# Performance work log

Hardware: AMD Instinct MI355X
Metric: run time of the kernel (lower is better)

The kernel has to match this reference:

```python
import jax, jax.numpy as jnp
import numpy as np

B, S, IN, D, H, L, M = 8, 1024, 256, 512, 8, 2, 64
DK = D // H
FF = 4 * D
EPS = 1e-5


def setup_inputs() -> dict:
    key = jax.random.key(0)
    ks = jax.random.split(key, 16)
    w = lambda k, shape: jax.random.normal(k, shape, jnp.float32) * 0.02
    return {
        "inputs": jax.random.normal(ks[0], (B, S, IN), jnp.float32),
        "lengths": jax.random.randint(ks[1], (B,), S // 2, S + 1),
        "W_in": w(ks[2], (IN, D)), "b_in": jnp.zeros((D,), jnp.float32),
        # per-layer stacked params (leading axis L) for lax.scan
        "Wq": w(ks[3], (L, D, D)), "bq": jnp.zeros((L, D), jnp.float32),
        "Wk": w(ks[4], (L, D, D)), "bk": jnp.zeros((L, D), jnp.float32),
        "Wv": w(ks[5], (L, D, D)), "bv": jnp.zeros((L, D), jnp.float32),
        "Wo": w(ks[6], (L, D, D)), "bo": jnp.zeros((L, D), jnp.float32),
        "rel_bias": w(ks[7], (L, H, 2 * M - 1)),
        "W1": w(ks[8], (L, D, FF)), "b1": jnp.zeros((L, FF), jnp.float32),
        "W2": w(ks[9], (L, FF, D)), "b2": jnp.zeros((L, D), jnp.float32),
        "g1": jnp.ones((L, D), jnp.float32), "be1": jnp.zeros((L, D), jnp.float32),
        "g2": jnp.ones((L, D), jnp.float32), "be2": jnp.zeros((L, D), jnp.float32),
        "gf": jnp.ones((D,), jnp.float32), "bef": jnp.zeros((D,), jnp.float32),
    }


def _ln(x, g, b):
    m = jnp.mean(x, axis=-1, keepdims=True)
    v = jnp.mean(jnp.square(x - m), axis=-1, keepdims=True)
    return (x - m) * jax.lax.rsqrt(v + EPS) * g + b


def _sinusoid_pe(seq_len, d_model):
    pos = jnp.arange(seq_len, dtype=jnp.float32)[:, None]
    div = jnp.exp(jnp.arange(0, d_model, 2, dtype=jnp.float32) * (-np.log(10000.0) / d_model))
    pe = jnp.zeros((seq_len, d_model), jnp.float32)
    pe = pe.at[:, 0::2].set(jnp.sin(pos * div))
    pe = pe.at[:, 1::2].set(jnp.cos(pos * div))
    return pe


def _encoder(inputs, lengths, W_in, b_in, Wq, bq, Wk, bk, Wv, bv, Wo, bo,
             rel_bias, W1, b1, W2, b2, g1, be1, g2, be2, gf, bef):
    x = inputs @ W_in + b_in                      # (B,S,D)
    x = x + _sinusoid_pe(S, D)[None]
    pad = jnp.arange(S)[None, :] >= lengths[:, None]   # (B,S) True = padded key

    r = jnp.arange(S)
    rel_idx = jnp.clip(r[:, None] - r[None, :], -(M - 1), M - 1) + (M - 1)  # (S,S)
    scale = 1.0 / np.sqrt(DK)

    def layer(x, p):
        (wq, bq_, wk, bk_, wv, bv_, wo, bo_, rb, w1, b1_, w2, b2_, g1_, be1_, g2_, be2_) = p
        # --- self-attention sublayer (pre-norm) ---
        h = _ln(x, g1_, be1_)
        q = (h @ wq + bq_).reshape(B, S, H, DK).transpose(0, 2, 1, 3)  # (B,H,S,DK)
        k = (h @ wk + bk_).reshape(B, S, H, DK).transpose(0, 2, 1, 3)
        v = (h @ wv + bv_).reshape(B, S, H, DK).transpose(0, 2, 1, 3)
        scores = jnp.einsum('bhqd,bhkd->bhqk', q, k) * scale
        scores = scores + rb[:, rel_idx][None]            # (H,S,S) relative bias
        scores = jnp.where(pad[:, None, None, :], -jnp.inf, scores)
        attn = jax.nn.softmax(scores, axis=-1)
        o = jnp.einsum('bhqk,bhkd->bhqd', attn, v)
        o = o.transpose(0, 2, 1, 3).reshape(B, S, D) @ wo + bo_
        x = x + o
        # --- FFN sublayer (pre-norm) ---
        h = _ln(x, g2_, be2_)
        x = x + (jax.nn.relu(h @ w1 + b1_) @ w2 + b2_)
        return x, None

    stacked = (Wq, bq, Wk, bk, Wv, bv, Wo, bo, rel_bias, W1, b1, W2, b2, g1, be1, g2, be2)
    x, _ = jax.lax.scan(layer, x, stacked)
    return _ln(x, gf, bef)


def reference(inputs, lengths, W_in, b_in, Wq, bq, Wk, bk, Wv, bv, Wo, bo,
              rel_bias, W1, b1, W2, b2, g1, be1, g2, be2, gf, bef):
    return _encoder(inputs, lengths, W_in, b_in, Wq, bq, Wk, bk, Wv, bv, Wo, bo,
                    rel_bias, W1, b1, W2, b2, g1, be1, g2, be2, gf, bef)
```

## Files before the change

### kernel.cpp

```cpp
#include <hip/hip_runtime.h>
#include <hip/hip_bf16.h>

typedef unsigned short u16;
typedef unsigned int u32;
typedef __bf16 v8bf __attribute__((ext_vector_type(8)));
typedef float v4f __attribute__((ext_vector_type(4)));

#define B_SZ 8
#define S_LEN 1024
#define IN_DIM 256
#define DMODEL 512
#define NHEAD 8
#define DK 64
#define FF_DIM 2048
#define MROWS (B_SZ * S_LEN)
#define QSCALE 0.1803368801111204f

__device__ __forceinline__ u16 f2bf(float f) {
    unsigned int x = __float_as_uint(f);
    unsigned int r = (x + 0x7fffu + ((x >> 16) & 1u)) >> 16;
    return (u16)r;
}

__device__ __forceinline__ void gl16(const u16* g, u16* l) {
    __builtin_amdgcn_global_load_lds((const __attribute__((address_space(1))) unsigned int*)g,
                                     (__attribute__((address_space(3))) unsigned int*)l, 16, 0, 0);
}

__global__ __launch_bounds__(256) void conv_bf16_kernel(const float* __restrict__ in,
                                                        u16* __restrict__ out, int n4) {
    int i = blockIdx.x * 256 + threadIdx.x;
    if (i < n4) {
        float4 v = ((const float4*)in)[i];
        ushort4 o;
        o.x = f2bf(v.x); o.y = f2bf(v.y); o.z = f2bf(v.z); o.w = f2bf(v.w);
        ((ushort4*)out)[i] = o;
    }
}

struct TDesc { const float* src; u16* dst; int K; int N; };
struct TArgs { TDesc d[13]; };

__global__ void transpose_conv_kernel(TArgs args) {
    TDesc t = args.d[blockIdx.z];
    int k0 = blockIdx.x * 32, n0 = blockIdx.y * 32;
    if (k0 >= t.K || n0 >= t.N) return;
    __shared__ float tile[32][33];
    int tx = threadIdx.x, ty = threadIdx.y;
#pragma unroll
    for (int j = 0; j < 4; j++) {
        int k = k0 + ty + j * 8;
        tile[ty + j * 8][tx] = t.src[(size_t)k * t.N + n0 + tx];
    }
    __syncthreads();
#pragma unroll
    for (int j = 0; j < 4; j++) {
        int n = n0 + ty + j * 8;
        t.dst[(size_t)n * t.K + k0 + tx] = f2bf(tile[tx][ty + j * 8]);
    }
}

template <bool OUT_BF16>
__global__ __launch_bounds__(256) void ln_kernel(const float* __restrict__ x,
                                                 const float* __restrict__ g,
                                                 const float* __restrict__ b,
                                                 void* __restrict__ out) {
    int row = blockIdx.x * 4 + (threadIdx.x >> 6);
    int lane = threadIdx.x & 63;
    const float4* xr = (const float4*)(x + (size_t)row * DMODEL);
    float4 v0 = xr[lane], v1 = xr[lane + 64];
    float s = v0.x + v0.y + v0.z + v0.w + v1.x + v1.y + v1.z + v1.w;
    float sq = v0.x * v0.x + v0.y * v0.y + v0.z * v0.z + v0.w * v0.w +
               v1.x * v1.x + v1.y * v1.y + v1.z * v1.z + v1.w * v1.w;
#pragma unroll
    for (int m = 1; m < 64; m <<= 1) {
        s += __shfl_xor(s, m);
        sq += __shfl_xor(sq, m);
    }
    float mean = s * (1.0f / DMODEL);
    float var = sq * (1.0f / DMODEL) - mean * mean;
    float rstd = rsqrtf(var + 1e-5f);
    const float4* g4 = (const float4*)g;
    const float4* b4 = (const float4*)b;
    float4 ga = g4[lane], gb = g4[lane + 64], ba = b4[lane], bb = b4[lane + 64];
    float4 r0, r1;
    r0.x = (v0.x - mean) * rstd * ga.x + ba.x;
    r0.y = (v0.y - mean) * rstd * ga.y + ba.y;
    r0.z = (v0.z - mean) * rstd * ga.z + ba.z;
    r0.w = (v0.w - mean) * rstd * ga.w + ba.w;
    r1.x = (v1.x - mean) * rstd * gb.x + bb.x;
    r1.y = (v1.y - mean) * rstd * gb.y + bb.y;
    r1.z = (v1.z - mean) * rstd * gb.z + bb.z;
    r1.w = (v1.w - mean) * rstd * gb.w + bb.w;
    if (OUT_BF16) {
        ushort4 o0, o1;
        o0.x = f2bf(r0.x); o0.y = f2bf(r0.y); o0.z = f2bf(r0.z); o0.w = f2bf(r0.w);
        o1.x = f2bf(r1.x); o1.y = f2bf(r1.y); o1.z = f2bf(r1.z); o1.w = f2bf(r1.w);
        ((ushort4*)out)[(size_t)row * 128 + lane] = o0;
        ((ushort4*)out)[(size_t)row * 128 + 64 + lane] = o1;
    } else {
        ((float4*)out)[(size_t)row * 128 + lane] = r0;
        ((float4*)out)[(size_t)row * 128 + 64 + lane] = r1;
    }
}

template <int MT, int NT>
__device__ __forceinline__ void gemm_core(const u16* __restrict__ A, const u16* __restrict__ Bt,
                                          int K, v4f (&acc)[MT][NT]) {
    constexpr int BM = MT * 32;
    constexpr int BN = NT * 32;
    __shared__ u16 As[BM * 64];
    __shared__ u16 Bs[BN * 64];
    int tid = threadIdx.x;
    int n0 = blockIdx.x * BN, m0 = blockIdx.y * BM;
    int w = tid >> 6, lane = tid & 63;
    int wr = (w >> 1) * (BM / 2), wc = (w & 1) * (BN / 2);
    int lr = lane & 15, lq = lane >> 4;
    int r8 = lane >> 3, cb = lane & 7;
    int scol = (cb ^ r8) * 8;

    v4f zero = {0.f, 0.f, 0.f, 0.f};
#pragma unroll
    for (int i = 0; i < MT; i++)
#pragma unroll
        for (int j = 0; j < NT; j++) acc[i][j] = zero;

    const u16* gA[MT]; u16* lA[MT];
#pragma unroll
    for (int j = 0; j < MT; j++) {
        int row0 = (MT * 8) * w + j * 8;
        gA[j] = A + (size_t)(m0 + row0 + r8) * K + scol;
        lA[j] = As + row0 * 64;
    }
    const u16* gB[NT]; u16* lB[NT];
#pragma unroll
    for (int j = 0; j < NT; j++) {
        int row0 = (NT * 8) * w + j * 8;
        gB[j] = Bt + (size_t)(n0 + row0 + r8) * K + scol;
        lB[j] = Bs + row0 * 64;
    }

    for (int k0 = 0; k0 < K; k0 += 64) {
#pragma unroll
        for (int j = 0; j < MT; j++) gl16(gA[j], lA[j]);
#pragma unroll
        for (int j = 0; j < NT; j++) gl16(gB[j], lB[j]);
        __syncthreads();
#pragma unroll
        for (int kk = 0; kk < 2; kk++) {
            int xb = ((kk * 4 + lq) ^ (lr & 7)) * 8;
            v8bf af[MT], bfr[NT];
#pragma unroll
            for (int i = 0; i < MT; i++)
                af[i] = *(const v8bf*)&As[(wr + i * 16 + lr) * 64 + xb];
#pragma unroll
            for (int j = 0; j < NT; j++)
                bfr[j] = *(const v8bf*)&Bs[(wc + j * 16 + lr) * 64 + xb];
#pragma unroll
            for (int mt = 0; mt < MT; mt++)
#pragma unroll
                for (int nt = 0; nt < NT; nt++)
                    acc[mt][nt] = __builtin_amdgcn_mfma_f32_16x16x32_bf16(af[mt], bfr[nt], acc[mt][nt], 0, 0, 0);
        }
        __syncthreads();
#pragma unroll
        for (int j = 0; j < MT; j++) gA[j] += 64;
#pragma unroll
        for (int j = 0; j < NT; j++) gB[j] += 64;
    }
}

__global__ __launch_bounds__(256) void gemm_in_kernel(const u16* __restrict__ A,
                                                      const u16* __restrict__ Bt,
                                                      const float* __restrict__ bias,
                                                      float* __restrict__ Out, int K) {
    v4f acc[4][2];
    gemm_core<4, 2>(A, Bt, K, acc);
    int tid = threadIdx.x, w = tid >> 6, lane = tid & 63;
    int lr = lane & 15, lq = lane >> 4;
    int wr = (w >> 1) * 64, wc = (w & 1) * 32;
    int n0 = blockIdx.x * 64, m0 = blockIdx.y * 128;
#pragma unroll
    for (int mt = 0; mt < 4; mt++) {
#pragma unroll
        for (int nt = 0; nt < 2; nt++) {
            int col = n0 + wc + nt * 16 + lr;
            float bcol = bias[col];
            float freq = __builtin_amdgcn_exp2f((float)(col & ~1) * (-0.025953277f));
#pragma unroll
            for (int reg = 0; reg < 4; reg++) {
                int row = m0 + wr + mt * 16 + lq * 4 + reg;
                float rev = (float)(row & (S_LEN - 1)) * freq * 0.15915494309189535f;
                float fr = __builtin_amdgcn_fractf(rev);
                float pe = (col & 1) ? __builtin_amdgcn_cosf(fr) : __builtin_amdgcn_sinf(fr);
                Out[(size_t)row * DMODEL + col] = acc[mt][nt][reg] + bcol + pe;
            }
        }
    }
}

__global__ __launch_bounds__(256) void gemm_qkv_kernel(const u16* __restrict__ A,
                                                       const u16* __restrict__ Bt,
                                                       const float* __restrict__ bq,
                                                       const float* __restrict__ bk,
                                                       const float* __restrict__ bv,
                                                       u16* __restrict__ Qo,
                                                       u16* __restrict__ Ko,
                                                       u16* __restrict__ Vto, int K) {
    v4f acc[4][4];
    gemm_core<4, 4>(A, Bt, K, acc);
    int tid = threadIdx.x, w = tid >> 6, lane = tid & 63;
    int lr = lane & 15, lq = lane >> 4;
    int wr = (w >> 1) * 64, wc = (w & 1) * 64;
    int n0 = blockIdx.x * 128, m0 = blockIdx.y * 128;
    int seg = n0 >> 9;
#pragma unroll
    for (int mt = 0; mt < 4; mt++) {
#pragma unroll
        for (int nt = 0; nt < 4; nt++) {
            int col = (n0 + wc + nt * 16 + lr) & (DMODEL - 1);
            if (seg == 0) {
                float bcol = bq[col];
#pragma unroll
                for (int reg = 0; reg < 4; reg++) {
                    int row = m0 + wr + mt * 16 + lq * 4 + reg;
                    Qo[(size_t)row * DMODEL + col] = f2bf((acc[mt][nt][reg] + bcol) * QSCALE);
                }
            } else if (seg == 1) {
                float bcol = bk[col];
#pragma unroll
                for (int reg = 0; reg < 4; reg++) {
                    int row = m0 + wr + mt * 16 + lq * 4 + reg;
                    Ko[(size_t)row * DMODEL + col] = f2bf(acc[mt][nt][reg] + bcol);
                }
            } else {
                float bcol = bv[col];
                int row0 = m0 + wr + mt * 16 + lq * 4;
                int bb = row0 >> 10, s0 = row0 & (S_LEN - 1);
                ushort4 o;
                o.x = f2bf(acc[mt][nt][0] + bcol);
                o.y = f2bf(acc[mt][nt][1] + bcol);
                o.z = f2bf(acc[mt][nt][2] + bcol);
                o.w = f2bf(acc[mt][nt][3] + bcol);
                *(ushort4*)(Vto + ((size_t)(bb * DMODEL + col)) * S_LEN + s0) = o;
            }
        }
    }
}

__global__ __launch_bounds__(256) void gemm_relu_kernel(const u16* __restrict__ A,
                                                        const u16* __restrict__ Bt,
                                                        const float* __restrict__ bias,
                                                        u16* __restrict__ Out, int N, int K) {
    v4f acc[4][4];
    gemm_core<4, 4>(A, Bt, K, acc);
    int tid = threadIdx.x, w = tid >> 6, lane = tid & 63;
    int lr = lane & 15, lq = lane >> 4;
    int wr = (w >> 1) * 64, wc = (w & 1) * 64;
    int n0 = blockIdx.x * 128, m0 = blockIdx.y * 128;
#pragma unroll
    for (int mt = 0; mt < 4; mt++) {
#pragma unroll
        for (int nt = 0; nt < 4; nt++) {
            int col = n0 + wc + nt * 16 + lr;
            float bcol = bias[col];
#pragma unroll
            for (int reg = 0; reg < 4; reg++) {
                int row = m0 + wr + mt * 16 + lq * 4 + reg;
                Out[(size_t)row * N + col] = f2bf(fmaxf(acc[mt][nt][reg] + bcol, 0.0f));
            }
        }
    }
}

__global__ __launch_bounds__(256) void gemm_res_kernel(const u16* __restrict__ A,
                                                       const u16* __restrict__ Bt,
                                                       const float* __restrict__ bias,
                                                       float* __restrict__ Out, int K) {
    v4f acc[4][2];
    gemm_core<4, 2>(A, Bt, K, acc);
    int tid = threadIdx.x, w = tid >> 6, lane = tid & 63;
    int lr = lane & 15, lq = lane >> 4;
    int wr = (w >> 1) * 64, wc = (w & 1) * 32;
    int n0 = blockIdx.x * 64, m0 = blockIdx.y * 128;
#pragma unroll
    for (int mt = 0; mt < 4; mt++) {
#pragma unroll
        for (int nt = 0; nt < 2; nt++) {
            int col = n0 + wc + nt * 16 + lr;
            float bcol = bias[col];
#pragma unroll
            for (int reg = 0; reg < 4; reg++) {
                int row = m0 + wr + mt * 16 + lq * 4 + reg;
                size_t idx = (size_t)row * DMODEL + col;
                Out[idx] = Out[idx] + acc[mt][nt][reg] + bcol;
            }
        }
    }
}

__global__ __launch_bounds__(256, 4) void fattn_kernel(const u16* __restrict__ Qg,
                                                       const u16* __restrict__ Kg,
                                                       const u16* __restrict__ Vtg,
                                                       const float* __restrict__ rb,
                                                       const int* __restrict__ lengths,
                                                       u16* __restrict__ Op,
                                                       float* __restrict__ lsums) {
    int bid = blockIdx.x;
    int wg = (bid & 7) * 128 + (bid >> 3);
    int i = wg & 127;
    int h = wg >> 7;
    int b = i & 7;
    int qt = (i >> 3) & 7;
    int kvh = (i >> 6) & 1;
    int tid = threadIdx.x, w = tid >> 6, lane = tid & 63;
    int lr = lane & 15, lq = lane >> 4;
    __shared__ u16 Ks[3][64 * 64];
    __shared__ u16 Vs[3][64 * 64];
    __shared__ float rbs[128];
    int len = lengths[b];
    if (tid < 127) rbs[tid] = rb[h * 127 + tid] * 1.4426950408889634f;

    int l2 = ((len + 127) >> 7) << 6;
    int kstart = kvh ? l2 : 0;
    int kend = kvh ? len : l2;
    int nchunks = (kend - kstart + 63) >> 6;

    int qw = qt * 128 + w * 32;
    v8bf qa[2][2];
#pragma unroll
    for (int ntq = 0; ntq < 2; ntq++) {
        size_t qrow = ((size_t)(b * S_LEN + qw + ntq * 16 + lr)) * DMODEL + h * DK;
        qa[ntq][0] = *(const v8bf*)(Qg + qrow + lq * 8);
        qa[ntq][1] = *(const v8bf*)(Qg + qrow + 32 + lq * 8);
    }

    v4f zero = {0.f, 0.f, 0.f, 0.f};
    v4f Oacc[4][2];
#pragma unroll
    for (int dt = 0; dt < 4; dt++)
#pragma unroll
        for (int nt = 0; nt < 2; nt++) Oacc[dt][nt] = zero;
    float lsum[2] = {0.f, 0.f};

    const u16* Kbase = Kg + ((size_t)b * S_LEN) * DMODEL + h * DK;
    const u16* Vbase = Vtg + ((size_t)(b * DMODEL + h * DK)) * S_LEN;
    int r8 = lane >> 3, cb = lane & 7;
    int swz = (cb ^ r8) * 8;

#pragma unroll
    for (int j = 0; j < 2; j++) {
        int row0 = w * 16 + j * 8;
        gl16(Kbase + (size_t)(kstart + row0 + r8) * DMODEL + swz, Ks[0] + row0 * 64);
        gl16(Vbase + (size_t)(row0 + r8) * S_LEN + kstart + swz, Vs[0] + row0 * 64);
    }
#pragma unroll
    for (int j = 0; j < 2; j++) {
        int row0 = w * 16 + j * 8;
        gl16(Kbase + (size_t)(kstart + 64 + row0 + r8) * DMODEL + swz, Ks[1] + row0 * 64);
        gl16(Vbase + (size_t)(row0 + r8) * S_LEN + kstart + 64 + swz, Vs[1] + row0 * 64);
    }
    __syncthreads();

    u16 *KsA = Ks[0], *VsA = Vs[0];
    u16 *KsB = Ks[1], *VsB = Vs[1];
    u16 *KsC = Ks[2], *VsC = Vs[2];

    for (int ci = 0; ci < nchunks; ci++) {
        int kb0 = kstart + ci * 64;
        if (ci > 0) {
            if (ci + 1 < nchunks) asm volatile("s_waitcnt vmcnt(4)" ::: "memory");
            else                  asm volatile("s_waitcnt vmcnt(0)" ::: "memory");
            __builtin_amdgcn_s_barrier();
            __builtin_amdgcn_sched_barrier(0);
        }
        if (ci + 2 < nchunks) {
            int nk = kb0 + 128;
#pragma unroll
            for (int j = 0; j < 2; j++) {
                int row0 = w * 16 + j * 8;
                gl16(Kbase + (size_t)(nk + row0 + r8) * DMODEL + swz, KsC + row0 * 64);
                gl16(Vbase + (size_t)(row0 + r8) * S_LEN + nk + swz, VsC + row0 * 64);
            }
        }
        const u16* Ksc = KsA;
        const u16* Vsc = VsA;

        v4f S[4][2];
        __builtin_amdgcn_s_setprio(1);
#pragma unroll
        for (int mtk = 0; mtk < 4; mtk++) {
            int xb0 = (lq ^ (lr & 7)) * 8;
            int xb1 = ((4 + lq) ^ (lr & 7)) * 8;
            v8bf kf0 = *(const v8bf*)&Ksc[(mtk * 16 + lr) * 64 + xb0];
            v8bf kf1 = *(const v8bf*)&Ksc[(mtk * 16 + lr) * 64 + xb1];
#pragma unroll
            for (int ntq = 0; ntq < 2; ntq++) {
                v4f s = __builtin_amdgcn_mfma_f32_16x16x32_bf16(kf0, qa[ntq][0], zero, 0, 0, 0);
                S[mtk][ntq] = __builtin_amdgcn_mfma_f32_16x16x32_bf16(kf1, qa[ntq][1], s, 0, 0, 0);
            }
        }
        __builtin_amdgcn_s_setprio(0);

        bool edge = (kb0 + 64 > len);
        int dmin = qw - (kb0 + 63), dmax = qw + 31 - kb0;
        bool perel = !(dmax <= -63 || dmin >= 63);
        float bconst = (dmax <= -63) ? rbs[0] : rbs[126];
        uint2 pks[4][2];
#pragma unroll
        for (int mtk = 0; mtk < 4; mtk++) {
#pragma unroll
            for (int ntq = 0; ntq < 2; ntq++) {
                int q = qw + ntq * 16 + lr;
                float p[4];
#pragma unroll
                for (int r = 0; r < 4; r++) {
                    int key = kb0 + mtk * 16 + lq * 4 + r;
                    float s = S[mtk][ntq][r];
                    if (perel) {
                        int d = q - key;
                        d = d < -63 ? -63 : (d > 63 ? 63 : d);
                        s += rbs[d + 63];
                    } else {
                        s += bconst;
                    }
                    float pv = __builtin_amdgcn_exp2f(s);
                    if (edge && key >= len) pv = 0.f;
                    lsum[ntq] += pv;
                    p[r] = pv;
                }
                pks[mtk][ntq].x = (__float_as_uint(p[1]) & 0xffff0000u) | (__float_as_uint(p[0]) >> 16);
                pks[mtk][ntq].y = (__float_as_uint(p[3]) & 0xffff0000u) | (__float_as_uint(p[2]) >> 16);
            }
        }

        __builtin_amdgcn_s_setprio(1);
#pragma unroll
        for (int kh = 0; kh < 2; kh++) {
            uint4 tp0 = {pks[kh * 2][0].x, pks[kh * 2][0].y, pks[kh * 2 + 1][0].x, pks[kh * 2 + 1][0].y};
            uint4 tp1 = {pks[kh * 2][1].x, pks[kh * 2][1].y, pks[kh * 2 + 1][1].x, pks[kh * 2 + 1][1].y};
            v8bf pb0 = *(v8bf*)&tp0;
            v8bf pb1 = *(v8bf*)&tp1;
            int gl = kh * 4 + (lq >> 1);
            int sub = (lq & 1) * 4;
#pragma unroll
            for (int dt = 0; dt < 4; dt++) {
                int drow = (dt * 16 + lr) * 64;
                uint2 lo = *(const uint2*)&Vsc[drow + ((gl ^ (lr & 7)) * 8 + sub)];
                uint2 hi = *(const uint2*)&Vsc[drow + (((gl + 2) ^ (lr & 7)) * 8 + sub)];
                uint4 tv = {lo.x, lo.y, hi.x, hi.y};
                v8bf va = *(v8bf*)&tv;
                Oacc[dt][0] = __builtin_amdgcn_mfma_f32_16x16x32_bf16(va, pb0, Oacc[dt][0], 0, 0, 0);
                Oacc[dt][1] = __builtin_amdgcn_mfma_f32_16x16x32_bf16(va, pb1, Oacc[dt][1], 0, 0, 0);
            }
        }
        __builtin_amdgcn_s_setprio(0);

        u16* t;
        t = KsA; KsA = KsB; KsB = KsC; KsC = t;
        t = VsA; VsA = VsB; VsB = VsC; VsC = t;
    }

    float lsumR[2];
#pragma unroll
    for (int ntq = 0; ntq < 2; ntq++) {
        float s = lsum[ntq];
        s += __shfl_xor(s, 16);
        s += __shfl_xor(s, 32);
        lsumR[ntq] = s;
    }
    if (lq == 0) {
#pragma unroll
        for (int ntq = 0; ntq < 2; ntq++) {
            int q = qw + ntq * 16 + lr;
            lsums[((size_t)kvh * MROWS + b * S_LEN + q) * NHEAD + h] = lsumR[ntq];
        }
    }
    u16* Oh = Op + (size_t)kvh * MROWS * DMODEL;
#pragma unroll
    for (int dt = 0; dt < 4; dt++) {
#pragma unroll
        for (int ntq = 0; ntq < 2; ntq++) {
            size_t off = (size_t)(b * S_LEN + qw + ntq * 16 + lr) * DMODEL + h * DK + dt * 16 + lq * 4;
            ushort4 o;
            o.x = f2bf(Oacc[dt][ntq][0]);
            o.y = f2bf(Oacc[dt][ntq][1]);
            o.z = f2bf(Oacc[dt][ntq][2]);
            o.w = f2bf(Oacc[dt][ntq][3]);
            *(ushort4*)(Oh + off) = o;
        }
    }
}

__device__ __forceinline__ u32 comb2(u32 a, u32 b, float inv) {
    float r0 = (__uint_as_float(a << 16) + __uint_as_float(b << 16)) * inv;
    float r1 = (__uint_as_float(a & 0xffff0000u) + __uint_as_float(b & 0xffff0000u)) * inv;
    return (u32)f2bf(r0) | ((u32)f2bf(r1) << 16);
}

__global__ __launch_bounds__(256) void attn_combine_kernel(const u16* __restrict__ Op,
                                                           const float* __restrict__ lsums,
                                                           u16* __restrict__ out) {
    int row = blockIdx.x * 4 + (threadIdx.x >> 6);
    int lane = threadIdx.x & 63;
    int h = lane >> 3;
    float l0 = lsums[(size_t)row * NHEAD + h];
    float l1 = lsums[((size_t)MROWS + row) * NHEAD + h];
    float inv = 1.0f / (l0 + l1);
    size_t base = (size_t)row * DMODEL + lane * 8;
    uint4 a = *(const uint4*)(Op + base);
    uint4 c = *(const uint4*)(Op + (size_t)MROWS * DMODEL + base);
    uint4 o;
    o.x = comb2(a.x, c.x, inv);
    o.y = comb2(a.y, c.y, inv);
    o.z = comb2(a.z, c.z, inv);
    o.w = comb2(a.w, c.w, inv);
    *(uint4*)(out + base) = o;
}

extern "C" void kernel_launch(void* const* d_in, const int* in_sizes, int n_in,
                              void* d_out, int out_size, void* d_ws, size_t ws_size,
                              hipStream_t stream) {
    const float* inputs   = (const float*)d_in[0];
    const int*   lengths  = (const int*)d_in[1];
    const float* W_in     = (const float*)d_in[2];
    const float* b_in     = (const float*)d_in[3];
    const float* Wq       = (const float*)d_in[4];
    const float* bq       = (const float*)d_in[5];
    const float* Wk       = (const float*)d_in[6];
    const float* bk       = (const float*)d_in[7];
    const float* Wv       = (const float*)d_in[8];
    const float* bv       = (const float*)d_in[9];
    const float* Wo       = (const float*)d_in[10];
    const float* bo       = (const float*)d_in[11];
    const float* rel_bias = (const float*)d_in[12];
    const float* W1       = (const float*)d_in[13];
    const float* b1       = (const float*)d_in[14];
    const float* W2       = (const float*)d_in[15];
    const float* b2       = (const float*)d_in[16];
    const float* g1       = (const float*)d_in[17];
    const float* be1      = (const float*)d_in[18];
    const float* g2       = (const float*)d_in[19];
    const float* be2      = (const float*)d_in[20];
    const float* gf       = (const float*)d_in[21];
    const float* bef      = (const float*)d_in[22];

    char* ws = (char*)d_ws;
    float* xbuf = (float*)ws;          ws += (size_t)MROWS * DMODEL * 4;
    u16* hbuf   = (u16*)ws;            ws += (size_t)MROWS * DMODEL * 2;
    u16* aobuf  = hbuf;
    u16* qbf    = (u16*)ws;            ws += (size_t)MROWS * FF_DIM * 2;
    u16* kbf    = qbf + (size_t)MROWS * DMODEL;
    u16* vtbf   = kbf + (size_t)MROWS * DMODEL;
    float* lsums = (float*)(vtbf + (size_t)MROWS * DMODEL);
    u16* tbuf   = qbf;
    u16* inbf   = qbf;
    u16* opart  = (u16*)d_out;
    u16* wt_in  = (u16*)ws;            ws += (size_t)DMODEL * IN_DIM * 2;
    u16 *qkvw[2], *wto[2], *wt1[2], *wt2[2];
    for (int l = 0; l < 2; l++) { qkvw[l] = (u16*)ws; ws += (size_t)3 * DMODEL * DMODEL * 2; }
    for (int l = 0; l < 2; l++) { wto[l] = (u16*)ws; ws += (size_t)DMODEL * DMODEL * 2; }
    for (int l = 0; l < 2; l++) { wt1[l] = (u16*)ws; ws += (size_t)FF_DIM * DMODEL * 2; }
    for (int l = 0; l < 2; l++) { wt2[l] = (u16*)ws; ws += (size_t)DMODEL * FF_DIM * 2; }

    TArgs ta;
    int ti = 0;
    ta.d[ti++] = {W_in, wt_in, IN_DIM, DMODEL};
    for (int l = 0; l < 2; l++) {
        ta.d[ti++] = {Wq + (size_t)l * DMODEL * DMODEL, qkvw[l], DMODEL, DMODEL};
        ta.d[ti++] = {Wk + (size_t)l * DMODEL * DMODEL, qkvw[l] + (size_t)DMODEL * DMODEL, DMODEL, DMODEL};
        ta.d[ti++] = {Wv + (size_t)l * DMODEL * DMODEL, qkvw[l] + (size_t)2 * DMODEL * DMODEL, DMODEL, DMODEL};
        ta.d[ti++] = {Wo + (size_t)l * DMODEL * DMODEL, wto[l], DMODEL, DMODEL};
        ta.d[ti++] = {W1 + (size_t)l * DMODEL * FF_DIM, wt1[l], DMODEL, FF_DIM};
        ta.d[ti++] = {W2 + (size_t)l * FF_DIM * DMODEL, wt2[l], FF_DIM, DMODEL};
    }

    conv_bf16_kernel<<<dim3((MROWS * IN_DIM / 4 + 255) / 256), 256, 0, stream>>>(
        inputs, inbf, MROWS * IN_DIM / 4);
    transpose_conv_kernel<<<dim3(64, 64, 13), dim3(32, 8), 0, stream>>>(ta);

    gemm_in_kernel<<<dim3(DMODEL / 64, MROWS / 128), 256, 0, stream>>>(
        inbf, wt_in, b_in, xbuf, IN_DIM);

    for (int l = 0; l < 2; l++) {
        ln_kernel<true><<<MROWS / 4, 256, 0, stream>>>(xbuf, g1 + l * DMODEL, be1 + l * DMODEL, hbuf);
        gemm_qkv_kernel<<<dim3(3 * DMODEL / 128, MROWS / 128), 256, 0, stream>>>(
            hbuf, qkvw[l], bq + l * DMODEL, bk + l * DMODEL, bv + l * DMODEL,
            qbf, kbf, vtbf, DMODEL);
        fattn_kernel<<<dim3(1024), 256, 0, stream>>>(
            qbf, kbf, vtbf, rel_bias + (size_t)l * NHEAD * 127, lengths, opart, lsums);
        attn_combine_kernel<<<MROWS / 4, 256, 0, stream>>>(opart, lsums, aobuf);
        gemm_res_kernel<<<dim3(DMODEL / 64, MROWS / 128), 256, 0, stream>>>(
            aobuf, wto[l], bo + l * DMODEL, xbuf, DMODEL);
        ln_kernel<true><<<MROWS / 4, 256, 0, stream>>>(xbuf, g2 + l * DMODEL, be2 + l * DMODEL, hbuf);
        gemm_relu_kernel<<<dim3(FF_DIM / 128, MROWS / 128), 256, 0, stream>>>(
            hbuf, wt1[l], b1 + l * FF_DIM, tbuf, FF_DIM, DMODEL);
        gemm_res_kernel<<<dim3(DMODEL / 64, MROWS / 128), 256, 0, stream>>>(
            tbuf, wt2[l], b2 + l * DMODEL, xbuf, FF_DIM);
    }
    ln_kernel<false><<<MROWS / 4, 256, 0, stream>>>(xbuf, gf, bef, d_out);
}
```

Baseline: 468.3 us.

## Drop split-KV attention and combine kernel; compact transpose grid

The attention kernel no longer splits the key range into two halves with a separate combine pass. Each workgroup now covers all keys and normalizes its output directly, which removes the combine kernel launch and the partial-output and lsum traffic. The cost is half as many workgroups (512) with longer, unevenly sized loops, so load balance and occupancy may suffer. The weight transpose launch also changes from a mostly idle 3D grid to a flat grid of only the valid tiles, found by a per-block search over start offsets.

```diff
diff --git a/kernel.cpp b/kernel.cpp
--- a/kernel.cpp
+++ b/kernel.cpp
@@ -39,12 +39,17 @@
 }
 
 struct TDesc { const float* src; u16* dst; int K; int N; };
-struct TArgs { TDesc d[13]; };
+struct TArgs { TDesc d[13]; int start[14]; int l2tn[13]; };
 
 __global__ void transpose_conv_kernel(TArgs args) {
-    TDesc t = args.d[blockIdx.z];
-    int k0 = blockIdx.x * 32, n0 = blockIdx.y * 32;
-    if (k0 >= t.K || n0 >= t.N) return;
+    int bid = blockIdx.x;
+    int z = 0;
+    while (z < 12 && bid >= args.start[z + 1]) z++;
+    TDesc t = args.d[z];
+    int local = bid - args.start[z];
+    int l2 = args.l2tn[z];
+    int k0 = (local >> l2) << 5;
+    int n0 = (local & ((1 << l2) - 1)) << 5;
     __shared__ float tile[32][33];
     int tx = threadIdx.x, ty = threadIdx.y;
 #pragma unroll
@@ -304,15 +309,13 @@
                                                        const u16* __restrict__ Vtg,
                                                        const float* __restrict__ rb,
                                                        const int* __restrict__ lengths,
-                                                       u16* __restrict__ Op,
-                                                       float* __restrict__ lsums) {
+                                                       u16* __restrict__ O) {
     int bid = blockIdx.x;
-    int wg = (bid & 7) * 128 + (bid >> 3);
-    int i = wg & 127;
-    int h = wg >> 7;
+    int wg = (bid & 7) * 64 + (bid >> 3);
+    int i = wg & 63;
+    int h = wg >> 6;
     int b = i & 7;
     int qt = (i >> 3) & 7;
-    int kvh = (i >> 6) & 1;
     int tid = threadIdx.x, w = tid >> 6, lane = tid & 63;
     int lr = lane & 15, lq = lane >> 4;
     __shared__ u16 Ks[3][64 * 64];
@@ -321,10 +324,7 @@
     int len = lengths[b];
     if (tid < 127) rbs[tid] = rb[h * 127 + tid] * 1.4426950408889634f;
 
-    int l2 = ((len + 127) >> 7) << 6;
-    int kstart = kvh ? l2 : 0;
-    int kend = kvh ? len : l2;
-    int nchunks = (kend - kstart + 63) >> 6;
+    int nchunks = (len + 63) >> 6;
 
     int qw = qt * 128 + w * 32;
     v8bf qa[2][2];
@@ -351,14 +351,14 @@
 #pragma unroll
     for (int j = 0; j < 2; j++) {
         int row0 = w * 16 + j * 8;
-        gl16(Kbase + (size_t)(kstart + row0 + r8) * DMODEL + swz, Ks[0] + row0 * 64);
-        gl16(Vbase + (size_t)(row0 + r8) * S_LEN + kstart + swz, Vs[0] + row0 * 64);
+        gl16(Kbase + (size_t)(row0 + r8) * DMODEL + swz, Ks[0] + row0 * 64);
+        gl16(Vbase + (size_t)(row0 + r8) * S_LEN + swz, Vs[0] + row0 * 64);
     }
 #pragma unroll
     for (int j = 0; j < 2; j++) {
         int row0 = w * 16 + j * 8;
-        gl16(Kbase + (size_t)(kstart + 64 + row0 + r8) * DMODEL + swz, Ks[1] + row0 * 64);
-        gl16(Vbase + (size_t)(row0 + r8) * S_LEN + kstart + 64 + swz, Vs[1] + row0 * 64);
+        gl16(Kbase + (size_t)(64 + row0 + r8) * DMODEL + swz, Ks[1] + row0 * 64);
+        gl16(Vbase + (size_t)(row0 + r8) * S_LEN + 64 + swz, Vs[1] + row0 * 64);
     }
     __syncthreads();
 
@@ -367,7 +367,7 @@
     u16 *KsC = Ks[2], *VsC = Vs[2];
 
     for (int ci = 0; ci < nchunks; ci++) {
-        int kb0 = kstart + ci * 64;
+        int kb0 = ci * 64;
         if (ci > 0) {
             if (ci + 1 < nchunks) asm volatile("s_waitcnt vmcnt(4)" ::: "memory");
             else                  asm volatile("s_waitcnt vmcnt(0)" ::: "memory");
@@ -461,61 +461,27 @@
         t = VsA; VsA = VsB; VsB = VsC; VsC = t;
     }
 
-    float lsumR[2];
+    float inv[2];
 #pragma unroll
     for (int ntq = 0; ntq < 2; ntq++) {
         float s = lsum[ntq];
         s += __shfl_xor(s, 16);
         s += __shfl_xor(s, 32);
-        lsumR[ntq] = s;
-    }
-    if (lq == 0) {
-#pragma unroll
-        for (int ntq = 0; ntq < 2; ntq++) {
-            int q = qw + ntq * 16 + lr;
-            lsums[((size_t)kvh * MROWS + b * S_LEN + q) * NHEAD + h] = lsumR[ntq];
-        }
-    }
-    u16* Oh = Op + (size_t)kvh * MROWS * DMODEL;
+        inv[ntq] = 1.0f / s;
+    }
 #pragma unroll
     for (int dt = 0; dt < 4; dt++) {
 #pragma unroll
         for (int ntq = 0; ntq < 2; ntq++) {
             size_t off = (size_t)(b * S_LEN + qw + ntq * 16 + lr) * DMODEL + h * DK + dt * 16 + lq * 4;
             ushort4 o;
-            o.x = f2bf(Oacc[dt][ntq][0]);
-            o.y = f2bf(Oacc[dt][ntq][1]);
-            o.z = f2bf(Oacc[dt][ntq][2]);
-            o.w = f2bf(Oacc[dt][ntq][3]);
-            *(ushort4*)(Oh + off) = o;
-        }
-    }
-}
-
-__device__ __forceinline__ u32 comb2(u32 a, u32 b, float inv) {
-    float r0 = (__uint_as_float(a << 16) + __uint_as_float(b << 16)) * inv;
-    float r1 = (__uint_as_float(a & 0xffff0000u) + __uint_as_float(b & 0xffff0000u)) * inv;
-    return (u32)f2bf(r0) | ((u32)f2bf(r1) << 16);
-}
-
-__global__ __launch_bounds__(256) void attn_combine_kernel(const u16* __restrict__ Op,
-                                                           const float* __restrict__ lsums,
-                                                           u16* __restrict__ out) {
-    int row = blockIdx.x * 4 + (threadIdx.x >> 6);
-    int lane = threadIdx.x & 63;
-    int h = lane >> 3;
-    float l0 = lsums[(size_t)row * NHEAD + h];
-    float l1 = lsums[((size_t)MROWS + row) * NHEAD + h];
-    float inv = 1.0f / (l0 + l1);
-    size_t base = (size_t)row * DMODEL + lane * 8;
-    uint4 a = *(const uint4*)(Op + base);
-    uint4 c = *(const uint4*)(Op + (size_t)MROWS * DMODEL + base);
-    uint4 o;
-    o.x = comb2(a.x, c.x, inv);
-    o.y = comb2(a.y, c.y, inv);
-    o.z = comb2(a.z, c.z, inv);
-    o.w = comb2(a.w, c.w, inv);
-    *(uint4*)(out + base) = o;
+            o.x = f2bf(Oacc[dt][ntq][0] * inv[ntq]);
+            o.y = f2bf(Oacc[dt][ntq][1] * inv[ntq]);
+            o.z = f2bf(Oacc[dt][ntq][2] * inv[ntq]);
+            o.w = f2bf(Oacc[dt][ntq][3] * inv[ntq]);
+            *(ushort4*)(O + off) = o;
+        }
+    }
 }
 
 extern "C" void kernel_launch(void* const* d_in, const int* in_sizes, int n_in,
@@ -552,10 +518,8 @@
     u16* qbf    = (u16*)ws;            ws += (size_t)MROWS * FF_DIM * 2;
     u16* kbf    = qbf + (size_t)MROWS * DMODEL;
     u16* vtbf   = kbf + (size_t)MROWS * DMODEL;
-    float* lsums = (float*)(vtbf + (size_t)MROWS * DMODEL);
     u16* tbuf   = qbf;
     u16* inbf   = qbf;
-    u16* opart  = (u16*)d_out;
     u16* wt_in  = (u16*)ws;            ws += (size_t)DMODEL * IN_DIM * 2;
     u16 *qkvw[2], *wto[2], *wt1[2], *wt2[2];
     for (int l = 0; l < 2; l++) { qkvw[l] = (u16*)ws; ws += (size_t)3 * DMODEL * DMODEL * 2; }
@@ -564,20 +528,30 @@
     for (int l = 0; l < 2; l++) { wt2[l] = (u16*)ws; ws += (size_t)DMODEL * FF_DIM * 2; }
 
     TArgs ta;
-    int ti = 0;
-    ta.d[ti++] = {W_in, wt_in, IN_DIM, DMODEL};
+    int ti = 0, acct = 0;
+    auto add = [&](const float* s, u16* d, int K, int N) {
+        ta.d[ti] = {s, d, K, N};
+        ta.start[ti] = acct;
+        int tn = N / 32;
+        int l2 = 31 - __builtin_clz((unsigned)tn);
+        ta.l2tn[ti] = l2;
+        acct += (K / 32) * tn;
+        ti++;
+    };
+    add(W_in, wt_in, IN_DIM, DMODEL);
     for (int l = 0; l < 2; l++) {
-        ta.d[ti++] = {Wq + (size_t)l * DMODEL * DMODEL, qkvw[l], DMODEL, DMODEL};
-        ta.d[ti++] = {Wk + (size_t)l * DMODEL * DMODEL, qkvw[l] + (size_t)DMODEL * DMODEL, DMODEL, DMODEL};
-        ta.d[ti++] = {Wv + (size_t)l * DMODEL * DMODEL, qkvw[l] + (size_t)2 * DMODEL * DMODEL, DMODEL, DMODEL};
-        ta.d[ti++] = {Wo + (size_t)l * DMODEL * DMODEL, wto[l], DMODEL, DMODEL};
-        ta.d[ti++] = {W1 + (size_t)l * DMODEL * FF_DIM, wt1[l], DMODEL, FF_DIM};
-        ta.d[ti++] = {W2 + (size_t)l * FF_DIM * DMODEL, wt2[l], FF_DIM, DMODEL};
-    }
+        add(Wq + (size_t)l * DMODEL * DMODEL, qkvw[l], DMODEL, DMODEL);
+        add(Wk + (size_t)l * DMODEL * DMODEL, qkvw[l] + (size_t)DMODEL * DMODEL, DMODEL, DMODEL);
+        add(Wv + (size_t)l * DMODEL * DMODEL, qkvw[l] + (size_t)2 * DMODEL * DMODEL, DMODEL, DMODEL);
+        add(Wo + (size_t)l * DMODEL * DMODEL, wto[l], DMODEL, DMODEL);
+        add(W1 + (size_t)l * DMODEL * FF_DIM, wt1[l], DMODEL, FF_DIM);
+        add(W2 + (size_t)l * FF_DIM * DMODEL, wt2[l], FF_DIM, DMODEL);
+    }
+    ta.start[13] = acct;
 
     conv_bf16_kernel<<<dim3((MROWS * IN_DIM / 4 + 255) / 256), 256, 0, stream>>>(
         inputs, inbf, MROWS * IN_DIM / 4);
-    transpose_conv_kernel<<<dim3(64, 64, 13), dim3(32, 8), 0, stream>>>(ta);
+    transpose_conv_kernel<<<dim3(acct), dim3(32, 8), 0, stream>>>(ta);
 
     gemm_in_kernel<<<dim3(DMODEL / 64, MROWS / 128), 256, 0, stream>>>(
         inbf, wt_in, b_in, xbuf, IN_DIM);
@@ -587,9 +561,8 @@
         gemm_qkv_kernel<<<dim3(3 * DMODEL / 128, MROWS / 128), 256, 0, stream>>>(
             hbuf, qkvw[l], bq + l * DMODEL, bk + l * DMODEL, bv + l * DMODEL,
             qbf, kbf, vtbf, DMODEL);
-        fattn_kernel<<<dim3(1024), 256, 0, stream>>>(
-            qbf, kbf, vtbf, rel_bias + (size_t)l * NHEAD * 127, lengths, opart, lsums);
-        attn_combine_kernel<<<MROWS / 4, 256, 0, stream>>>(opart, lsums, aobuf);
+        fattn_kernel<<<dim3(512), 256, 0, stream>>>(
+            qbf, kbf, vtbf, rel_bias + (size_t)l * NHEAD * 127, lengths, aobuf);
         gemm_res_kernel<<<dim3(DMODEL / 64, MROWS / 128), 256, 0, stream>>>(
             aobuf, wto[l], bo + l * DMODEL, xbuf, DMODEL);
         ln_kernel<true><<<MROWS / 4, 256, 0, stream>>>(xbuf, g2 + l * DMODEL, be2 + l * DMODEL, hbuf);
```

New measurement: 444.8 us. -5.0%, faster.
